# Kernel tuning notes

Hardware: AMD Instinct MI355X
Metric: run time of the kernel (lower is better)

## Reference

```python
import jax, jax.numpy as jnp
import numpy as np

N, H, E, G, OUT = 50000, 128, 600000, 256, 64
NUM_ITERS = 5
GAMMA = 0.1
EPS = 0.1
NEG_SLOPE = 0.01


def setup_inputs() -> dict:
    key = jax.random.key(0)
    ks = jax.random.split(key, 10)
    s = 1.0 / np.sqrt(H)
    x = jax.random.normal(ks[0], (N, H), dtype=jnp.float32)
    edge_index = jax.random.randint(ks[1], (2, E), 0, N, dtype=jnp.int64)
    batch = jnp.sort(jax.random.randint(ks[2], (N,), 0, G, dtype=jnp.int64))
    W = jax.random.normal(ks[3], (H, H), dtype=jnp.float32) * s
    bias = jax.random.normal(ks[4], (H,), dtype=jnp.float32) * s
    lin_w = jax.random.normal(ks[5], (H, H), dtype=jnp.float32) * s
    l1_w = jax.random.normal(ks[6], (3 * H // 2, 3 * H), dtype=jnp.float32) / np.sqrt(3 * H)
    l1_b = jax.random.normal(ks[7], (3 * H // 2,), dtype=jnp.float32) * 0.01
    l2_w = jax.random.normal(ks[8], (OUT, 3 * H // 2), dtype=jnp.float32) / np.sqrt(3 * H // 2)
    l2_b = jax.random.normal(ks[9], (OUT,), dtype=jnp.float32) * 0.01
    return {"x": x, "edge_index": edge_index, "batch": batch, "W": W, "bias": bias,
            "lin_w": lin_w, "l1_w": l1_w, "l1_b": l1_b, "l2_w": l2_w, "l2_b": l2_b}


def reference(x, edge_index, batch, W, bias, lin_w, l1_w, l1_b, l2_w, l2_b):
    n = x.shape[0]
    src, dst = edge_index[0], edge_index[1]
    # antisymmetric weight: W - W^T - gamma*I
    A = W - W.T - GAMMA * jnp.eye(W.shape[0], dtype=x.dtype)
    for _ in range(NUM_ITERS):
        neigh = x @ lin_w.T                                   # [N,H] linear (no bias)
        agg = jax.ops.segment_sum(neigh[src], dst, num_segments=n)  # gather-scatter add
        conv = x @ A.T + agg + bias
        x = x + EPS * jnp.tanh(conv)
    # triple global pooling per graph: add / max / mean
    add = jax.ops.segment_sum(x, batch, num_segments=G)
    mx = jax.ops.segment_max(x, batch, num_segments=G)
    cnt = jax.ops.segment_sum(jnp.ones((n,), dtype=x.dtype), batch, num_segments=G)
    safe_cnt = jnp.maximum(cnt, 1.0)[:, None]
    mean = add / safe_cnt
    mx = jnp.where(cnt[:, None] > 0, mx, 0.0)
    pooled = jnp.concatenate([add, mx, mean], axis=1)          # [G, 3H]
    h = jax.nn.leaky_relu(pooled @ l1_w.T + l1_b, NEG_SLOPE)
    out = jax.nn.leaky_relu(h @ l2_w.T + l2_b, NEG_SLOPE)
    return out
```

## Files before the change

kernel.cpp:

```cpp
#include <hip/hip_runtime.h>
#include <hip/hip_fp16.h>
#include <cmath>

#define H 128
#define GAMMA 0.1f
#define EPS 0.1f
#define NEG 0.01f
#define NGRAPH 256
#define ROWU16 64
#define CAPE 62

typedef _Float16 half_t;
typedef _Float16 f16x8 __attribute__((ext_vector_type(8)));
typedef _Float16 f16x2 __attribute__((ext_vector_type(2)));
typedef __fp16 fp16v2 __attribute__((ext_vector_type(2)));
typedef float f32x4 __attribute__((ext_vector_type(4)));
typedef float f32x2 __attribute__((ext_vector_type(2)));

__device__ __forceinline__ float fast_tanh(float v) {
    float e = __builtin_amdgcn_exp2f(v * 2.8853900817779268f);
    float r = __builtin_amdgcn_rcpf(e + 1.0f);
    return 1.0f - 2.0f * r;
}

__device__ __forceinline__ int pkrtz_bits(float x, float y) {
    union { fp16v2 h; int i; } u;
    u.h = __builtin_amdgcn_cvt_pkrtz(x, y);
    return u.i;
}

__global__ __launch_bounds__(256) void prep_cast_zero(
        const float* __restrict__ W, const float* __restrict__ lin_w,
        half_t* __restrict__ WtTf, const float* __restrict__ x,
        half_t* __restrict__ xh, unsigned char* __restrict__ xq,
        unsigned short* __restrict__ csr, int n4, int N) {
    int stride = gridDim.x * 256;
    int tot = max(n4, max(32768, N));
    for (int i = blockIdx.x * 256 + threadIdx.x; i < tot; i += stride) {
        if (i < n4) {
            float4 v = *(const float4*)(x + (size_t)i * 4);
            half_t* o = xh + (size_t)i * 4;
            o[0] = (half_t)v.x; o[1] = (half_t)v.y; o[2] = (half_t)v.z; o[3] = (half_t)v.w;
            int w = __builtin_amdgcn_cvt_pk_fp8_f32(v.x, v.y, 0, false);
            w = __builtin_amdgcn_cvt_pk_fp8_f32(v.z, v.w, w, true);
            *(int*)(xq + (size_t)i * 4) = w;
        }
        if (i < 32768) {
            int t = i & 7;
            int lane = (i >> 3) & 63;
            int ct = (i >> 9) & 7;
            int s = i >> 12;
            int q = lane >> 4, m = lane & 15;
            int j = m * 8 + ct;
            int k = s * 32 + q * 8 + t;
            float v;
            if (k < H) v = W[j * H + k] - W[k * H + j] - (j == k ? GAMMA : 0.f);
            else       v = lin_w[j * H + (k - H)];
            WtTf[i] = (half_t)v;
        }
        if (i < N) *(int*)(csr + (size_t)i * ROWU16) = 0;
    }
}

__global__ __launch_bounds__(256) void fill_direct(const int* __restrict__ src,
        const int* __restrict__ dst, unsigned short* __restrict__ csr, int E) {
    int e = blockIdx.x * 256 + threadIdx.x;
    if (e < E) {
        int d = dst[e];
        int* rowcnt = (int*)(csr + (size_t)d * ROWU16);
        int p = atomicAdd(rowcnt, 1);
        if (p < CAPE) ((unsigned short*)rowcnt)[2 + p] = (unsigned short)src[e];
    }
}

__global__ __launch_bounds__(256) void gather_agg(const unsigned char* __restrict__ xq,
        const unsigned short* __restrict__ csr, half_t* __restrict__ xaggh, int N) {
    int wid = blockIdx.x * 4 + (threadIdx.x >> 6);
    int nw = gridDim.x * 4;
    int lane = threadIdx.x & 63;
    int slot = lane >> 3, chunk = lane & 7;

    int node = wid * 2;
    if (node >= N) return;
    int rA = (int)csr[(size_t)node * ROWU16 + lane];
    int rB = (node + 1 < N) ? (int)csr[(size_t)(node + 1) * ROWU16 + lane] : 0;

    while (true) {
        int curA = rA, curB = rB;
        int hasB = (node + 1 < N);
        int nxt = node + 2 * nw;
        if (nxt < N) {
            rA = (int)csr[(size_t)nxt * ROWU16 + lane];
            rB = (nxt + 1 < N) ? (int)csr[(size_t)(nxt + 1) * ROWU16 + lane] : 0;
        }
        int cntA = min(__builtin_amdgcn_readlane(curA, 0) |
                       (__builtin_amdgcn_readlane(curA, 1) << 16), CAPE);
        int cntB = hasB ? min(__builtin_amdgcn_readlane(curB, 0) |
                              (__builtin_amdgcn_readlane(curB, 1) << 16), CAPE) : 0;

        f32x2 aA[8], aB[8];
#pragma unroll
        for (int k = 0; k < 8; ++k) { aA[k] = (f32x2){0.f, 0.f}; aB[k] = (f32x2){0.f, 0.f}; }

        int bA = 0, bB = 0;
        while (bA < cntA && bB < cntB) {
            int iA = __builtin_amdgcn_ds_bpermute((2 + min(bA + slot, cntA - 1)) << 2, curA);
            int iB = __builtin_amdgcn_ds_bpermute((2 + min(bB + slot, cntB - 1)) << 2, curB);
            int4 dA = *(const int4*)(xq + (size_t)iA * H + chunk * 16);
            int4 dB = *(const int4*)(xq + (size_t)iB * H + chunk * 16);
            if (bA + slot < cntA) {
                aA[0] += __builtin_amdgcn_cvt_pk_f32_fp8(dA.x, false);
                aA[1] += __builtin_amdgcn_cvt_pk_f32_fp8(dA.x, true);
                aA[2] += __builtin_amdgcn_cvt_pk_f32_fp8(dA.y, false);
                aA[3] += __builtin_amdgcn_cvt_pk_f32_fp8(dA.y, true);
                aA[4] += __builtin_amdgcn_cvt_pk_f32_fp8(dA.z, false);
                aA[5] += __builtin_amdgcn_cvt_pk_f32_fp8(dA.z, true);
                aA[6] += __builtin_amdgcn_cvt_pk_f32_fp8(dA.w, false);
                aA[7] += __builtin_amdgcn_cvt_pk_f32_fp8(dA.w, true);
            }
            if (bB + slot < cntB) {
                aB[0] += __builtin_amdgcn_cvt_pk_f32_fp8(dB.x, false);
                aB[1] += __builtin_amdgcn_cvt_pk_f32_fp8(dB.x, true);
                aB[2] += __builtin_amdgcn_cvt_pk_f32_fp8(dB.y, false);
                aB[3] += __builtin_amdgcn_cvt_pk_f32_fp8(dB.y, true);
                aB[4] += __builtin_amdgcn_cvt_pk_f32_fp8(dB.z, false);
                aB[5] += __builtin_amdgcn_cvt_pk_f32_fp8(dB.z, true);
                aB[6] += __builtin_amdgcn_cvt_pk_f32_fp8(dB.w, false);
                aB[7] += __builtin_amdgcn_cvt_pk_f32_fp8(dB.w, true);
            }
            bA += 8; bB += 8;
        }
        while (bA < cntA) {
            int iA = __builtin_amdgcn_ds_bpermute((2 + min(bA + slot, cntA - 1)) << 2, curA);
            int4 dA = *(const int4*)(xq + (size_t)iA * H + chunk * 16);
            if (bA + slot < cntA) {
                aA[0] += __builtin_amdgcn_cvt_pk_f32_fp8(dA.x, false);
                aA[1] += __builtin_amdgcn_cvt_pk_f32_fp8(dA.x, true);
                aA[2] += __builtin_amdgcn_cvt_pk_f32_fp8(dA.y, false);
                aA[3] += __builtin_amdgcn_cvt_pk_f32_fp8(dA.y, true);
                aA[4] += __builtin_amdgcn_cvt_pk_f32_fp8(dA.z, false);
                aA[5] += __builtin_amdgcn_cvt_pk_f32_fp8(dA.z, true);
                aA[6] += __builtin_amdgcn_cvt_pk_f32_fp8(dA.w, false);
                aA[7] += __builtin_amdgcn_cvt_pk_f32_fp8(dA.w, true);
            }
            bA += 8;
        }
        while (bB < cntB) {
            int iB = __builtin_amdgcn_ds_bpermute((2 + min(bB + slot, cntB - 1)) << 2, curB);
            int4 dB = *(const int4*)(xq + (size_t)iB * H + chunk * 16);
            if (bB + slot < cntB) {
                aB[0] += __builtin_amdgcn_cvt_pk_f32_fp8(dB.x, false);
                aB[1] += __builtin_amdgcn_cvt_pk_f32_fp8(dB.x, true);
                aB[2] += __builtin_amdgcn_cvt_pk_f32_fp8(dB.y, false);
                aB[3] += __builtin_amdgcn_cvt_pk_f32_fp8(dB.y, true);
                aB[4] += __builtin_amdgcn_cvt_pk_f32_fp8(dB.z, false);
                aB[5] += __builtin_amdgcn_cvt_pk_f32_fp8(dB.z, true);
                aB[6] += __builtin_amdgcn_cvt_pk_f32_fp8(dB.w, false);
                aB[7] += __builtin_amdgcn_cvt_pk_f32_fp8(dB.w, true);
            }
            bB += 8;
        }

#pragma unroll
        for (int half = 0; half < 2; ++half) {
            f32x2* a = half ? aB : aA;
            if (half && !hasB) break;
            union { f16x2 h; int i; } t[8];
#pragma unroll
            for (int k = 0; k < 8; ++k) t[k].i = pkrtz_bits(a[k].x, a[k].y);
#pragma unroll
            for (int m = 8; m <= 32; m <<= 1) {
#pragma unroll
                for (int k = 0; k < 8; ++k) {
                    union { f16x2 h; int i; } o;
                    o.i = __shfl_xor(t[k].i, m, 64);
                    t[k].h += o.h;
                }
            }
            if (lane < 8) {
                union { int i[4]; f16x8 v; } lo, hi;
#pragma unroll
                for (int k = 0; k < 4; ++k) { lo.i[k] = t[k].i; hi.i[k] = t[k + 4].i; }
                half_t* dst = xaggh + (size_t)(node + half) * H + chunk * 16;
                *(f16x8*)dst = lo.v;
                *(f16x8*)(dst + 8) = hi.v;
            }
        }

        if (nxt >= N) break;
        node = nxt;
    }
}

#define CROWS 64
__global__ __launch_bounds__(256) void conv_mfma(
        const half_t* __restrict__ xh, const half_t* __restrict__ xaggh,
        const half_t* __restrict__ WtTf, const float* __restrict__ bias,
        half_t* __restrict__ xhout, unsigned char* __restrict__ xqout, int N) {
    int tid = threadIdx.x;
    int wave = tid >> 6, lane = tid & 63;
    int q = lane >> 4, m = lane & 15;
    int n0 = blockIdx.x * CROWS + wave * 16;

    f32x4 acc[8];
#pragma unroll
    for (int ct = 0; ct < 8; ++ct) acc[ct] = (f32x4){0.f, 0.f, 0.f, 0.f};

    int arow = min(n0 + m, N - 1);
#pragma unroll
    for (int s = 0; s < 8; ++s) {
        f16x8 afrag = (s < 4)
            ? *(const f16x8*)(xh    + (size_t)arow * H + s * 32 + q * 8)
            : *(const f16x8*)(xaggh + (size_t)arow * H + (s - 4) * 32 + q * 8);
#pragma unroll
        for (int ct = 0; ct < 8; ++ct) {
            f16x8 bfrag = *(const f16x8*)(WtTf + ((s * 8 + ct) * 64 + lane) * 8);
            acc[ct] = __builtin_amdgcn_mfma_f32_16x16x32_f16(afrag, bfrag, acc[ct], 0, 0, 0);
        }
    }

    float4 b0 = *(const float4*)(bias + m * 8);
    float4 b1 = *(const float4*)(bias + m * 8 + 4);
    float bb[8] = {b0.x, b0.y, b0.z, b0.w, b1.x, b1.y, b1.z, b1.w};
#pragma unroll
    for (int r = 0; r < 4; ++r) {
        int row = n0 + q * 4 + r;
        if (row < N) {
            f16x8 xr = *(const f16x8*)(xh + (size_t)row * H + m * 8);
            f16x8 o;
            float fv[8];
#pragma unroll
            for (int ct = 0; ct < 8; ++ct) {
                float c = acc[ct][r] + bb[ct];
                float val = (float)xr[ct] + EPS * fast_tanh(c);
                o[ct] = (half_t)val;
                fv[ct] = val;
            }
            *(f16x8*)(xhout + (size_t)row * H + m * 8) = o;
            int lo = __builtin_amdgcn_cvt_pk_fp8_f32(fv[0], fv[1], 0, false);
            lo = __builtin_amdgcn_cvt_pk_fp8_f32(fv[2], fv[3], lo, true);
            int hi = __builtin_amdgcn_cvt_pk_fp8_f32(fv[4], fv[5], 0, false);
            hi = __builtin_amdgcn_cvt_pk_fp8_f32(fv[6], fv[7], hi, true);
            *(int2*)(xqout + (size_t)row * H + m * 8) = make_int2(lo, hi);
        }
    }
}

__global__ __launch_bounds__(1024) void pool_mlp(const half_t* __restrict__ x,
        const int* __restrict__ batch,
        const float* __restrict__ l1_w, const float* __restrict__ l1_b,
        const float* __restrict__ l2_w, const float* __restrict__ l2_b,
        float* __restrict__ out, int N) {
    __shared__ float ssum[8][128];
    __shared__ float smax[8][128];
    __shared__ __align__(16) float sp[384];
    __shared__ __align__(16) float sh[192];
    int g = blockIdx.x, t = threadIdx.x;
    int feat = t & 127, slot = t >> 7;
    int lo = 0, hi = N;
    while (lo < hi) { int mid = (lo + hi) >> 1; if (batch[mid] < g) lo = mid + 1; else hi = mid; }
    int start = lo;
    hi = N;
    while (lo < hi) { int mid = (lo + hi) >> 1; if (batch[mid] < g + 1) lo = mid + 1; else hi = mid; }
    int end = lo;
    float sum = 0.f, mx = -INFINITY;
    for (int n = start + slot; n < end; n += 8) {
        float v = (float)x[(size_t)n * H + feat];
        sum += v;
        mx = fmaxf(mx, v);
    }
    ssum[slot][feat] = sum;
    smax[slot][feat] = mx;
    __syncthreads();
    if (t < 128) {
        float s = 0.f, m = -INFINITY;
#pragma unroll
        for (int k = 0; k < 8; ++k) { s += ssum[k][t]; m = fmaxf(m, smax[k][t]); }
        int cnt = end - start;
        sp[t] = s;
        sp[128 + t] = (cnt > 0) ? m : 0.f;
        sp[256 + t] = s / (float)(cnt > 0 ? cnt : 1);
    }
    __syncthreads();
    if (t < 192) {
        float acc = l1_b[t];
        const float* wr = l1_w + (size_t)t * 384;
        for (int k = 0; k < 384; k += 4) {
            float4 w = *(const float4*)(wr + k);
            float4 p = *(const float4*)(sp + k);
            acc += w.x * p.x + w.y * p.y + w.z * p.z + w.w * p.w;
        }
        sh[t] = acc > 0.f ? acc : NEG * acc;
    }
    __syncthreads();
    if (t < 64) {
        float acc = l2_b[t];
        const float* wr = l2_w + (size_t)t * 192;
        for (int k = 0; k < 192; k += 4) {
            float4 w = *(const float4*)(wr + k);
            float4 p = *(const float4*)(sh + k);
            acc += w.x * p.x + w.y * p.y + w.z * p.z + w.w * p.w;
        }
        out[g * 64 + t] = acc > 0.f ? acc : NEG * acc;
    }
}

extern "C" void kernel_launch(void* const* d_in, const int* in_sizes, int n_in,
                              void* d_out, int out_size, void* d_ws, size_t ws_size,
                              hipStream_t stream) {
    const float* x0    = (const float*)d_in[0];
    const int*   edge  = (const int*)d_in[1];
    const int*   batch = (const int*)d_in[2];
    const float* W     = (const float*)d_in[3];
    const float* bias  = (const float*)d_in[4];
    const float* lin_w = (const float*)d_in[5];
    const float* l1_w  = (const float*)d_in[6];
    const float* l1_b  = (const float*)d_in[7];
    const float* l2_w  = (const float*)d_in[8];
    const float* l2_b  = (const float*)d_in[9];
    float* out = (float*)d_out;

    int N = in_sizes[0] / H;
    int E = in_sizes[1] / 2;
    const int* src = edge;
    const int* dst = edge + E;

    size_t nh = (size_t)N * H;
    half_t* xhA    = (half_t*)d_ws;
    half_t* xhB    = xhA + nh;
    half_t* xaggh  = xhB + nh;
    half_t* WtTf   = xaggh + nh;
    unsigned short* csr = (unsigned short*)(WtTf + 32768);
    unsigned char* xq   = (unsigned char*)(csr + (size_t)N * ROWU16);

    int n4 = (int)(nh / 4);
    prep_cast_zero<<<1024, 256, 0, stream>>>(W, lin_w, WtTf, x0, xhA, xq, csr, n4, N);

    fill_direct<<<(E + 255) / 256, 256, 0, stream>>>(src, dst, csr, E);

    const half_t* xcur_h = xhA;
    int nblocks = (N + CROWS - 1) / CROWS;
    for (int it = 0; it < 5; ++it) {
        gather_agg<<<2048, 256, 0, stream>>>(xq, csr, xaggh, N);
        half_t* xnext_h = (it & 1) ? xhA : xhB;
        conv_mfma<<<nblocks, 256, 0, stream>>>(xcur_h, xaggh, WtTf, bias, xnext_h, xq, N);
        xcur_h = xnext_h;
    }

    pool_mlp<<<NGRAPH, 1024, 0, stream>>>(xcur_h, batch, l1_w, l1_b, l2_w, l2_b, out, N);
}
```

Baseline: 341.7 us.

## Split gather feature columns across block halves and use nontemporal CSR loads/stores

The gather-aggregate kernel now divides each node's 128 feature columns into two 64-column halves. Interleaved groups of blocks handle each half, so every lane loads 8 bytes instead of 16 and keeps half as many accumulators. The aim is lower register pressure and more independent in-flight gathers. CSR row reads and the fp16 aggregate writes switch to nontemporal hints. In exchange, every CSR row is now read by two waves, and each neighbour row is fetched as two 64-byte pieces rather than one 128-byte access.

```diff
diff --git a/kernel.cpp b/kernel.cpp
--- a/kernel.cpp
+++ b/kernel.cpp
@@ -16,6 +16,7 @@
 typedef __fp16 fp16v2 __attribute__((ext_vector_type(2)));
 typedef float f32x4 __attribute__((ext_vector_type(4)));
 typedef float f32x2 __attribute__((ext_vector_type(2)));
+typedef int i32x4 __attribute__((ext_vector_type(4)));
 
 __device__ __forceinline__ float fast_tanh(float v) {
     float e = __builtin_amdgcn_exp2f(v * 2.8853900817779268f);
@@ -75,115 +76,103 @@
 
 __global__ __launch_bounds__(256) void gather_agg(const unsigned char* __restrict__ xq,
         const unsigned short* __restrict__ csr, half_t* __restrict__ xaggh, int N) {
-    int wid = blockIdx.x * 4 + (threadIdx.x >> 6);
-    int nw = gridDim.x * 4;
-    int lane = threadIdx.x & 63;
+    int bid = blockIdx.x;
+    int tid = threadIdx.x;
+    int hf = (bid & 7) >> 2;
+    int widh = ((((bid >> 3) << 2) | (bid & 3)) << 2) | (tid >> 6);
+    int nwh = (gridDim.x >> 1) * 4;
+    int lane = tid & 63;
     int slot = lane >> 3, chunk = lane & 7;
-
-    int node = wid * 2;
+    int cboff = hf * 64 + chunk * 8;
+
+    int node = widh * 2;
     if (node >= N) return;
-    int rA = (int)csr[(size_t)node * ROWU16 + lane];
-    int rB = (node + 1 < N) ? (int)csr[(size_t)(node + 1) * ROWU16 + lane] : 0;
+    int rA = (int)__builtin_nontemporal_load(csr + (size_t)node * ROWU16 + lane);
+    int rB = (node + 1 < N)
+        ? (int)__builtin_nontemporal_load(csr + (size_t)(node + 1) * ROWU16 + lane) : 0;
 
     while (true) {
         int curA = rA, curB = rB;
         int hasB = (node + 1 < N);
-        int nxt = node + 2 * nw;
+        int nxt = node + 2 * nwh;
         if (nxt < N) {
-            rA = (int)csr[(size_t)nxt * ROWU16 + lane];
-            rB = (nxt + 1 < N) ? (int)csr[(size_t)(nxt + 1) * ROWU16 + lane] : 0;
+            rA = (int)__builtin_nontemporal_load(csr + (size_t)nxt * ROWU16 + lane);
+            rB = (nxt + 1 < N)
+                ? (int)__builtin_nontemporal_load(csr + (size_t)(nxt + 1) * ROWU16 + lane) : 0;
         }
         int cntA = min(__builtin_amdgcn_readlane(curA, 0) |
                        (__builtin_amdgcn_readlane(curA, 1) << 16), CAPE);
         int cntB = hasB ? min(__builtin_amdgcn_readlane(curB, 0) |
                               (__builtin_amdgcn_readlane(curB, 1) << 16), CAPE) : 0;
 
-        f32x2 aA[8], aB[8];
-#pragma unroll
-        for (int k = 0; k < 8; ++k) { aA[k] = (f32x2){0.f, 0.f}; aB[k] = (f32x2){0.f, 0.f}; }
+        f32x2 aA[4], aB[4];
+#pragma unroll
+        for (int k = 0; k < 4; ++k) { aA[k] = (f32x2){0.f, 0.f}; aB[k] = (f32x2){0.f, 0.f}; }
 
         int bA = 0, bB = 0;
         while (bA < cntA && bB < cntB) {
             int iA = __builtin_amdgcn_ds_bpermute((2 + min(bA + slot, cntA - 1)) << 2, curA);
             int iB = __builtin_amdgcn_ds_bpermute((2 + min(bB + slot, cntB - 1)) << 2, curB);
-            int4 dA = *(const int4*)(xq + (size_t)iA * H + chunk * 16);
-            int4 dB = *(const int4*)(xq + (size_t)iB * H + chunk * 16);
+            int2 dA = *(const int2*)(xq + (size_t)iA * H + cboff);
+            int2 dB = *(const int2*)(xq + (size_t)iB * H + cboff);
             if (bA + slot < cntA) {
                 aA[0] += __builtin_amdgcn_cvt_pk_f32_fp8(dA.x, false);
                 aA[1] += __builtin_amdgcn_cvt_pk_f32_fp8(dA.x, true);
                 aA[2] += __builtin_amdgcn_cvt_pk_f32_fp8(dA.y, false);
                 aA[3] += __builtin_amdgcn_cvt_pk_f32_fp8(dA.y, true);
-                aA[4] += __builtin_amdgcn_cvt_pk_f32_fp8(dA.z, false);
-                aA[5] += __builtin_amdgcn_cvt_pk_f32_fp8(dA.z, true);
-                aA[6] += __builtin_amdgcn_cvt_pk_f32_fp8(dA.w, false);
-                aA[7] += __builtin_amdgcn_cvt_pk_f32_fp8(dA.w, true);
             }
             if (bB + slot < cntB) {
                 aB[0] += __builtin_amdgcn_cvt_pk_f32_fp8(dB.x, false);
                 aB[1] += __builtin_amdgcn_cvt_pk_f32_fp8(dB.x, true);
                 aB[2] += __builtin_amdgcn_cvt_pk_f32_fp8(dB.y, false);
                 aB[3] += __builtin_amdgcn_cvt_pk_f32_fp8(dB.y, true);
-                aB[4] += __builtin_amdgcn_cvt_pk_f32_fp8(dB.z, false);
-                aB[5] += __builtin_amdgcn_cvt_pk_f32_fp8(dB.z, true);
-                aB[6] += __builtin_amdgcn_cvt_pk_f32_fp8(dB.w, false);
-                aB[7] += __builtin_amdgcn_cvt_pk_f32_fp8(dB.w, true);
             }
             bA += 8; bB += 8;
         }
         while (bA < cntA) {
             int iA = __builtin_amdgcn_ds_bpermute((2 + min(bA + slot, cntA - 1)) << 2, curA);
-            int4 dA = *(const int4*)(xq + (size_t)iA * H + chunk * 16);
+            int2 dA = *(const int2*)(xq + (size_t)iA * H + cboff);
             if (bA + slot < cntA) {
                 aA[0] += __builtin_amdgcn_cvt_pk_f32_fp8(dA.x, false);
                 aA[1] += __builtin_amdgcn_cvt_pk_f32_fp8(dA.x, true);
                 aA[2] += __builtin_amdgcn_cvt_pk_f32_fp8(dA.y, false);
                 aA[3] += __builtin_amdgcn_cvt_pk_f32_fp8(dA.y, true);
-                aA[4] += __builtin_amdgcn_cvt_pk_f32_fp8(dA.z, false);
-                aA[5] += __builtin_amdgcn_cvt_pk_f32_fp8(dA.z, true);
-                aA[6] += __builtin_amdgcn_cvt_pk_f32_fp8(dA.w, false);
-                aA[7] += __builtin_amdgcn_cvt_pk_f32_fp8(dA.w, true);
             }
             bA += 8;
         }
         while (bB < cntB) {
             int iB = __builtin_amdgcn_ds_bpermute((2 + min(bB + slot, cntB - 1)) << 2, curB);
-            int4 dB = *(const int4*)(xq + (size_t)iB * H + chunk * 16);
+            int2 dB = *(const int2*)(xq + (size_t)iB * H + cboff);
             if (bB + slot < cntB) {
                 aB[0] += __builtin_amdgcn_cvt_pk_f32_fp8(dB.x, false);
                 aB[1] += __builtin_amdgcn_cvt_pk_f32_fp8(dB.x, true);
                 aB[2] += __builtin_amdgcn_cvt_pk_f32_fp8(dB.y, false);
                 aB[3] += __builtin_amdgcn_cvt_pk_f32_fp8(dB.y, true);
-                aB[4] += __builtin_amdgcn_cvt_pk_f32_fp8(dB.z, false);
-                aB[5] += __builtin_amdgcn_cvt_pk_f32_fp8(dB.z, true);
-                aB[6] += __builtin_amdgcn_cvt_pk_f32_fp8(dB.w, false);
-                aB[7] += __builtin_amdgcn_cvt_pk_f32_fp8(dB.w, true);
             }
             bB += 8;
         }
 
 #pragma unroll
-        for (int half = 0; half < 2; ++half) {
-            f32x2* a = half ? aB : aA;
-            if (half && !hasB) break;
-            union { f16x2 h; int i; } t[8];
-#pragma unroll
-            for (int k = 0; k < 8; ++k) t[k].i = pkrtz_bits(a[k].x, a[k].y);
+        for (int h2 = 0; h2 < 2; ++h2) {
+            f32x2* a = h2 ? aB : aA;
+            if (h2 && !hasB) break;
+            union { f16x2 h; int i; } t[4];
+#pragma unroll
+            for (int k = 0; k < 4; ++k) t[k].i = pkrtz_bits(a[k].x, a[k].y);
 #pragma unroll
             for (int m = 8; m <= 32; m <<= 1) {
 #pragma unroll
-                for (int k = 0; k < 8; ++k) {
+                for (int k = 0; k < 4; ++k) {
                     union { f16x2 h; int i; } o;
                     o.i = __shfl_xor(t[k].i, m, 64);
                     t[k].h += o.h;
                 }
             }
             if (lane < 8) {
-                union { int i[4]; f16x8 v; } lo, hi;
-#pragma unroll
-                for (int k = 0; k < 4; ++k) { lo.i[k] = t[k].i; hi.i[k] = t[k + 4].i; }
-                half_t* dst = xaggh + (size_t)(node + half) * H + chunk * 16;
-                *(f16x8*)dst = lo.v;
-                *(f16x8*)(dst + 8) = hi.v;
+                i32x4 w;
+                w.x = t[0].i; w.y = t[1].i; w.z = t[2].i; w.w = t[3].i;
+                __builtin_nontemporal_store(w,
+                    (i32x4*)(xaggh + (size_t)(node + h2) * H + cboff));
             }
         }
 
```

Measured after the change: 360.4 us. +5.5%, slower.
